# Optimization experiments

Hardware: AMD Instinct MI355X
Metric: run time of the kernel (lower is better)

## Reference

```python
import jax, jax.numpy as jnp
import numpy as np

BETA = 0.01
EPS = 1e-6

def conv3x3(x, w, b):
    y = jax.lax.conv_general_dilated(x, w, (1, 1), 'SAME',
                                     dimension_numbers=('NCHW', 'OIHW', 'NCHW'))
    return y + b[None, :, None, None]

def variance_depth_flow(gt, patch, max_depth):
    B, C, H, W = gt.shape
    py, px = H // patch, W // patch
    # [B,C,py,px,P,P]
    p = gt.reshape(B, C, py, patch, px, patch).transpose(0, 1, 2, 4, 3, 5)
    p = jnp.where((p > 0.1) & (p < max_depth), p, jnp.zeros_like(p))
    bn = jnp.log(p[..., 0, :] + EPS)   # north border  [B,C,py,px,P]
    bs = jnp.log(p[..., -1, :] + EPS)  # south
    bw = jnp.log(p[..., :, 0] + EPS)   # west
    be = jnp.log(p[..., :, -1] + EPS)  # east
    def sx(b):  # shift patches left along x (axis=3), zero-pad last column
        return jnp.concatenate([b[:, :, :, 1:], jnp.zeros_like(b[:, :, :, :1])], axis=3)
    def sy(b):  # shift patches up along y (axis=2), zero-pad last row
        return jnp.concatenate([b[:, :, 1:], jnp.zeros_like(b[:, :, :1])], axis=2)
    diffs = [be - sx(bw), bs - sy(bn), be - sx(be), bs - sy(bs), bw - sx(bw),
             bn - sy(bn), bs - sx(bs), be - sy(be), bn - sx(bn), bw - sy(bw)]
    d = jnp.stack([x.sum(-1) for x in diffs], axis=-1)  # [B,C,py,px,10]
    d = d[:, 0].transpose(0, 3, 1, 2) / patch            # [B,10,py,px]
    return d

def smooth_l1(pred, target, beta):
    d = pred - target
    ad = jnp.abs(d)
    return jnp.where(ad < beta, 0.5 * d * d / beta, ad - 0.5 * beta)

def setup_inputs() -> dict:
    key = jax.random.key(0)
    ks = jax.random.split(key, 7)
    B, FC, DC, hw, HW = 32, 256, 64, 64, 512
    feat = jax.random.normal(ks[0], (B, FC, hw, hw), dtype=jnp.float32)
    depth = jax.random.normal(ks[1], (B, DC, hw, hw), dtype=jnp.float32)
    gts = jax.random.uniform(ks[2], (B, 1, HW, HW), dtype=jnp.float32)
    W_att = jax.random.normal(ks[3], (DC, FC, 3, 3), dtype=jnp.float32) * 0.02
    b_att = jnp.zeros((DC,), dtype=jnp.float32)
    W_post = jax.random.normal(ks[4], (10, DC, 3, 3), dtype=jnp.float32) * 0.05
    b_post = jnp.zeros((10,), dtype=jnp.float32)
    return {"feat": feat, "depth": depth, "gts": gts,
            "W_att": W_att, "b_att": b_att, "W_post": W_post, "b_post": b_post}

def reference(feat, depth, gts, W_att, b_att, W_post, b_post):
    max_depth = 80.0
    n, c, h, w = depth.shape
    patch = gts.shape[2] // h
    flow_gradient = variance_depth_flow(gts, patch, max_depth)  # [B,10,h,w]
    att = jax.nn.sigmoid(conv3x3(feat, W_att, b_att))           # [B,DC,h,w]
    ds = conv3x3(att * depth, W_post, b_post)                   # [B,10,h,w]
    diff = smooth_l1(ds, flow_gradient, BETA)
    return diff.sum() / (h * w * ds.shape[0] * ds.shape[1])
```

## Files before the change

kernel.cpp:

```cpp
#include <hip/hip_runtime.h>
#include <hip/hip_bf16.h>


typedef __attribute__((ext_vector_type(4))) float f32x4;
typedef __attribute__((ext_vector_type(8))) short s16x8;

#define DEVFN __device__ __forceinline__

DEVFN float bf2f(unsigned short u){
  unsigned int x = ((unsigned int)u) << 16;
  float f; __builtin_memcpy(&f, &x, 4); return f;
}
DEVFN unsigned short f2bf(float f){
  unsigned int x; __builtin_memcpy(&x, &f, 4);
  x += 0x7fffu + ((x >> 16) & 1u);
  return (unsigned short)(x >> 16);
}

#define ASYNC16(gp, lp) __builtin_amdgcn_global_load_lds( \
    (const __attribute__((address_space(1))) unsigned int*)(gp), \
    (__attribute__((address_space(3))) unsigned int*)(lp), 16, 0, 0)

__global__ void k_weights(const float* __restrict__ Watt, const float* __restrict__ Wpost,
                          unsigned short* __restrict__ WT1, unsigned short* __restrict__ WT2){
  const int t = blockIdx.x * 256 + threadIdx.x;
  const int n1 = 9 * 64 * 256;
  if (t < n1){
    const int tap = t / (64 * 256);
    const int rem = t % (64 * 256);
    const int oc = rem / 256, ic = rem % 256;
    WT1[t] = f2bf(Watt[(oc * 256 + ic) * 9 + tap]);
  }
  const int n2 = 9 * 16 * 64;
  if (t < n2){
    const int tap = t / (16 * 64);
    const int rem = t % (16 * 64);
    const int od = rem / 64, ic = rem % 64;
    const float v = (od < 10) ? Wpost[(od * 64 + ic) * 9 + tap] : 0.0f;
    WT2[t] = f2bf(v);
  }
}

__global__ void k_borders(const float* __restrict__ gts, float* __restrict__ S,
                          float* __restrict__ out){
  const int bid = blockIdx.x, tid = threadIdx.x;
  if (bid == 0 && tid == 0) *out = 0.0f;
  __shared__ float slab[4096];
  const int rel = bid;
  const float* gp = gts + (size_t)rel * 4096;
#pragma unroll
  for (int it = 0; it < 4; ++it){
    const int id = it * 256 + tid;
    *(f32x4*)&slab[id * 4] = *(const f32x4*)&gp[id * 4];
  }
  __syncthreads();
  const int px = tid & 63, border = tid >> 6;
  float s = 0.0f;
#pragma unroll
  for (int i = 0; i < 8; ++i){
    float v;
    if (border == 0)      v = slab[px * 8 + i];
    else if (border == 1) v = slab[7 * 512 + px * 8 + i];
    else if (border == 2) v = slab[i * 512 + px * 8];
    else                  v = slab[i * 512 + px * 8 + 7];
    v = ((v > 0.1f) && (v < 80.0f)) ? v : 0.0f;
    s += __logf(v + 1e-6f);
  }
  S[((size_t)rel * 64 + px) * 4 + border] = s;
}

__global__ __launch_bounds__(256, 2) void k_gemm1(
    const float* __restrict__ feat,
    const unsigned short* __restrict__ WT1,
    const float* __restrict__ batt,
    const float* __restrict__ depth,
    unsigned short* __restrict__ adT)
{
  __shared__ unsigned short As[6 * 66 * 32];
  __shared__ unsigned short Bs[576 * 32];
  const int t = threadIdx.x;
  const int l = t & 63, w = t >> 6;
  const int b = blockIdx.x >> 4, ytile = blockIdx.x & 15;
  const int y0 = ytile * 4;
  const int fr = l & 15, g = l >> 4;
  const int x = l;

  f32x4 acc[4][4];
#pragma unroll
  for (int i = 0; i < 4; ++i)
#pragma unroll
    for (int j = 0; j < 4; ++j)
#pragma unroll
      for (int q = 0; q < 4; ++q) acc[i][j][q] = 0.0f;

  if (t < 48){
    const int yy = t >> 3, k = t & 7;
    const int xp = (k & 1) ? 65 : 0;
    s16x8 z = {0,0,0,0,0,0,0,0};
    *(s16x8*)&As[(yy * 66 + xp) * 32 + (k >> 1) * 8] = z;
  }

  const int xp = x + 1;
  const int sx = (xp >> 1) & 3;
  const int slotB = (g ^ ((fr >> 1) & 3)) * 8;

  for (int c = 0; c < 8; ++c){
    float rr[48];
#pragma unroll
    for (int j = 0; j < 6; ++j){
      const int yr = y0 - 1 + j;
      if (yr >= 0 && yr < 64){
        const float* gp = feat + ((size_t)(b * 256 + c * 32 + w * 8)) * 4096
                               + (size_t)yr * 64 + x;
#pragma unroll
        for (int e = 0; e < 8; ++e) rr[j * 8 + e] = gp[(size_t)e * 4096];
      } else {
#pragma unroll
        for (int e = 0; e < 8; ++e) rr[j * 8 + e] = 0.0f;
      }
    }
#pragma unroll
    for (int it = 0; it < 9; ++it){
      const int idx = it * 256 + t;
      const int row = idx >> 2;
      const int sg = (idx & 3) ^ ((row >> 1) & 3);
      ASYNC16(WT1 + (size_t)row * 256 + c * 32 + sg * 8, &Bs[(size_t)idx * 8]);
    }
#pragma unroll
    for (int j = 0; j < 6; ++j){
      s16x8 v;
#pragma unroll
      for (int e = 0; e < 8; ++e) v[e] = (short)f2bf(rr[j * 8 + e]);
      *(s16x8*)&As[(j * 66 + xp) * 32 + ((w ^ sx) * 8)] = v;
    }
    __syncthreads();

    for (int tap = 0; tap < 9; ++tap){
      const int dy = tap / 3 - 1, dxp = tap % 3;
      const int r = fr + dxp;
      const int slotA = (g ^ ((r >> 1) & 3)) * 8;
      const int rowb = ((w + dy + 1) * 66 + r) * 32 + slotA;
      s16x8 af[4], bfr[4];
#pragma unroll
      for (int i = 0; i < 4; ++i) af[i] = *(const s16x8*)&As[rowb + i * 512];
#pragma unroll
      for (int j = 0; j < 4; ++j)
        bfr[j] = *(const s16x8*)&Bs[(tap * 64 + j * 16 + fr) * 32 + slotB];
#pragma unroll
      for (int i = 0; i < 4; ++i)
#pragma unroll
        for (int j = 0; j < 4; ++j)
          acc[i][j] = __builtin_amdgcn_mfma_f32_16x16x32_bf16(af[i], bfr[j], acc[i][j], 0, 0, 0);
    }
    __syncthreads();
  }

  const int y = y0 + w;
#pragma unroll
  for (int j = 0; j < 4; ++j){
    const int oc = j * 16 + fr;
    const float bb = batt[oc];
    const float* dpt = depth + ((size_t)(b * 64 + oc)) * 4096 + (size_t)y * 64;
    unsigned short* op = adT + ((size_t)(b * 4096 + y * 64)) * 64 + oc;
#pragma unroll
    for (int i = 0; i < 4; ++i){
#pragma unroll
      for (int q = 0; q < 4; ++q){
        const int xo = i * 16 + g * 4 + q;
        const float v = acc[i][j][q] + bb;
        const float att = 1.0f / (1.0f + __expf(-v));
        op[(size_t)xo * 64] = f2bf(att * dpt[xo]);
      }
    }
  }
}

DEVFN float sel4(f32x4 v, int i){
  const float ab = (i & 1) ? v[1] : v[0];
  const float cd = (i & 1) ? v[3] : v[2];
  return (i & 2) ? cd : ab;
}

__global__ __launch_bounds__(512, 2) void k_gemm2(
    const unsigned short* __restrict__ adT,
    const unsigned short* __restrict__ WT2,
    const float* __restrict__ bpost,
    const f32x4* __restrict__ S,
    float* __restrict__ out)
{
  __shared__ unsigned short As[2][20480];
  __shared__ unsigned short Bs[9216];
  __shared__ float ps[8];
  const int t = threadIdx.x;
  const int l = t & 63, w = t >> 6;
  const int b = blockIdx.x >> 3, ytile = blockIdx.x & 7;
  const int y0 = ytile * 8;
  const int fr = l & 15, g = l >> 4;

  f32x4 acc[4];
#pragma unroll
  for (int i = 0; i < 4; ++i)
#pragma unroll
    for (int q = 0; q < 4; ++q) acc[i][q] = 0.0f;

  auto stageA = [&](int c, int d){
#pragma unroll
    for (int it2 = 0; it2 < 5; ++it2){
      const int it = it2 * 2 + (t >> 8);
      const int yy = y0 - 1 + it;
      const int xx = (t >> 2) & 63, icg = t & 3;
      unsigned short* lp = &As[d][(it * 64 + xx) * 32 + icg * 8];
      if (yy >= 0 && yy < 64){
        const int sg = icg ^ ((xx >> 1) & 3);
        const unsigned short* gp = adT
            + ((size_t)(b * 4096 + yy * 64 + xx)) * 64 + c * 32 + sg * 8;
        ASYNC16(gp, lp);
      } else {
        s16x8 z = {0,0,0,0,0,0,0,0};
        *(s16x8*)lp = z;
      }
    }
  };
#pragma unroll
  for (int it = 0; it < 3; ++it){
    const int idx = it * 512 + t;
    if (idx < 1152){
      const int row = idx >> 3, p = idx & 7;
      const int sg = p ^ (row & 7);
      ASYNC16(WT2 + (size_t)row * 64 + sg * 8, Bs + (size_t)idx * 8);
    }
  }
  stageA(0, 0);
  __syncthreads();

  for (int c = 0; c < 2; ++c){
    if (c == 0) stageA(1, 1);
    const unsigned short* Ab = As[c];
    const int pB = ((c * 4 + g) ^ (fr & 7)) * 8;
    for (int tap = 0; tap < 9; ++tap){
      const int dy = tap / 3 - 1, dx = tap % 3 - 1;
      s16x8 af[4];
#pragma unroll
      for (int i = 0; i < 4; ++i){
        const int xv = i * 16 + fr + dx;
        const bool valid = (xv >= 0) && (xv < 64);
        const int xw = valid ? xv : 0;
        const int slot = (g ^ ((xw >> 1) & 3)) * 8;
        s16x8 v = *(const s16x8*)&Ab[((w + dy + 1) * 64 + xw) * 32 + slot];
        s16x8 z = {0,0,0,0,0,0,0,0};
        af[i] = valid ? v : z;
      }
      const s16x8 bfr = *(const s16x8*)&Bs[(tap * 16 + fr) * 64 + pB];
#pragma unroll
      for (int i = 0; i < 4; ++i)
        acc[i] = __builtin_amdgcn_mfma_f32_16x16x32_bf16(af[i], bfr, acc[i], 0, 0, 0);
    }
    __syncthreads();
  }

  const unsigned aPack = (3u<<0)|(1u<<2)|(3u<<4)|(1u<<6)|(2u<<8)|(0u<<10)|(1u<<12)|(3u<<14)|(0u<<16)|(2u<<18);
  const unsigned bPack = (2u<<0)|(0u<<2)|(3u<<4)|(1u<<6)|(2u<<8)|(0u<<10)|(1u<<12)|(3u<<14)|(0u<<16)|(2u<<18);
  float lsum = 0.0f;
  const int y = y0 + w;
  if (fr < 10){
    const int od = fr;
    const int ai = (aPack >> (2 * od)) & 3;
    const int bi = (bPack >> (2 * od)) & 3;
    const bool xshift = (od & 1) == 0;
    const float bp = bpost[od];
#pragma unroll
    for (int i = 0; i < 4; ++i){
#pragma unroll
      for (int q = 0; q < 4; ++q){
        const int xo = i * 16 + g * 4 + q;
        const size_t gm = (size_t)b * 4096 + (size_t)y * 64 + xo;
        const f32x4 sa = S[gm];
        const bool nb = xshift ? (xo < 63) : (y < 63);
        const size_t ga = xshift ? (nb ? gm + 1 : gm) : (nb ? gm + 64 : gm);
        const f32x4 sbv = S[ga];
        const float sbf = nb ? sel4(sbv, bi) : 0.0f;
        const float flow = (sel4(sa, ai) - sbf) * 0.125f;
        const float dv = acc[i][q] + bp - flow;
        const float adv = fabsf(dv);
        lsum += (adv < 0.01f) ? (50.0f * dv * dv) : (adv - 0.005f);
      }
    }
  }
#pragma unroll
  for (int off = 32; off > 0; off >>= 1) lsum += __shfl_down(lsum, off);
  if (l == 0) ps[w] = lsum;
  __syncthreads();
  if (t == 0){
    float s = 0.0f;
#pragma unroll
    for (int i = 0; i < 8; ++i) s += ps[i];
    atomicAdd(out, s * (1.0f / 1310720.0f));
  }
}

extern "C" void kernel_launch(void* const* d_in, const int* in_sizes, int n_in,
                              void* d_out, int out_size, void* d_ws, size_t ws_size,
                              hipStream_t stream){
  const float* feat  = (const float*)d_in[0];
  const float* depth = (const float*)d_in[1];
  const float* gts   = (const float*)d_in[2];
  const float* Watt  = (const float*)d_in[3];
  const float* batt  = (const float*)d_in[4];
  const float* Wpost = (const float*)d_in[5];
  const float* bpost = (const float*)d_in[6];
  float* out = (float*)d_out;
  char* ws = (char*)d_ws;

  unsigned short* adT = (unsigned short*)ws;
  unsigned short* WT1 = (unsigned short*)(ws + 16777216);
  unsigned short* WT2 = (unsigned short*)(ws + 16777216 + 294912);
  float*          S   = (float*)(ws + 16777216 + 294912 + 18432);

  k_weights<<<576, 256, 0, stream>>>(Watt, Wpost, WT1, WT2);
  k_gemm1<<<512, 256, 0, stream>>>(feat, WT1, batt, depth, adT);
  k_borders<<<2048, 256, 0, stream>>>(gts, S, out);
  k_gemm2<<<256, 512, 0, stream>>>(adT, WT2, bpost, (const f32x4*)S, out);
}
```

Measured before the change: 90.16 us.

## Retile conv GEMM to 8-row tiles with split output channels and vectorized staging

Restructures k_gemm1 so each 512-thread block computes 8 output rows for half of the output channels (32), instead of 4 rows for all 64 channels. Input staging now uses float4 global loads and packed bf16 conversion via v_cvt_pk_bf16_f32 into a new XOR-swizzled LDS layout. The halo overhead per row drops from 6/4 to 10/8, and the per-thread accumulator count halves, which should allow higher occupancy. The cost is that feature-map staging is duplicated across the two channel-half blocks.

```diff
diff --git a/kernel.cpp b/kernel.cpp
--- a/kernel.cpp
+++ b/kernel.cpp
@@ -4,6 +4,7 @@
 
 typedef __attribute__((ext_vector_type(4))) float f32x4;
 typedef __attribute__((ext_vector_type(8))) short s16x8;
+typedef __attribute__((ext_vector_type(4))) unsigned int u32x4;
 
 #define DEVFN __device__ __forceinline__
 
@@ -15,6 +16,11 @@
   unsigned int x; __builtin_memcpy(&x, &f, 4);
   x += 0x7fffu + ((x >> 16) & 1u);
   return (unsigned short)(x >> 16);
+}
+DEVFN unsigned cvtpk(float lo, float hi){
+  unsigned r;
+  asm("v_cvt_pk_bf16_f32 %0, %1, %2" : "=v"(r) : "v"(lo), "v"(hi));
+  return r;
 }
 
 #define ASYNC16(gp, lp) __builtin_amdgcn_global_load_lds( \
@@ -69,87 +75,103 @@
   S[((size_t)rel * 64 + px) * 4 + border] = s;
 }
 
-__global__ __launch_bounds__(256, 2) void k_gemm1(
+__global__ __launch_bounds__(512, 4) void k_gemm1(
     const float* __restrict__ feat,
     const unsigned short* __restrict__ WT1,
     const float* __restrict__ batt,
     const float* __restrict__ depth,
     unsigned short* __restrict__ adT)
 {
-  __shared__ unsigned short As[6 * 66 * 32];
-  __shared__ unsigned short Bs[576 * 32];
+  __shared__ unsigned short As[10 * 33 * 64];
+  __shared__ unsigned short Bs[288 * 32];
   const int t = threadIdx.x;
   const int l = t & 63, w = t >> 6;
-  const int b = blockIdx.x >> 4, ytile = blockIdx.x & 15;
-  const int y0 = ytile * 4;
+  const int bid = blockIdx.x;
+  const int b = bid >> 4, ytile = (bid >> 1) & 7, oh = bid & 1;
+  const int y0 = ytile * 8, oc0 = oh * 32;
   const int fr = l & 15, g = l >> 4;
-  const int x = l;
-
-  f32x4 acc[4][4];
+
+  f32x4 acc[4][2];
 #pragma unroll
   for (int i = 0; i < 4; ++i)
 #pragma unroll
-    for (int j = 0; j < 4; ++j)
+    for (int j = 0; j < 2; ++j)
 #pragma unroll
       for (int q = 0; q < 4; ++q) acc[i][j][q] = 0.0f;
 
-  if (t < 48){
+  if (t < 80){
     const int yy = t >> 3, k = t & 7;
     const int xp = (k & 1) ? 65 : 0;
-    s16x8 z = {0,0,0,0,0,0,0,0};
-    *(s16x8*)&As[(yy * 66 + xp) * 32 + (k >> 1) * 8] = z;
-  }
-
-  const int xp = x + 1;
-  const int sx = (xp >> 1) & 3;
+    const int G = (k >> 1) & 3;
+    const int r = xp >> 1;
+    const int s = (4 * (xp & 1) + G) ^ (r & 7);
+    u32x4 z = {0, 0, 0, 0};
+    *(u32x4*)&As[(yy * 33 + r) * 64 + s * 8] = z;
+  }
+
+  auto stageRow = [&](int c, int yrow){
+    const int yr = y0 - 1 + yrow;
+    f32x4 v[8];
+    if (yr >= 0 && yr < 64){
+      const float* gp = feat + ((size_t)(b * 256 + c * 32 + g * 8)) * 4096
+                             + (size_t)yr * 64 + fr * 4;
+#pragma unroll
+      for (int e = 0; e < 8; ++e) v[e] = *(const f32x4*)(gp + (size_t)e * 4096);
+    } else {
+#pragma unroll
+      for (int e = 0; e < 8; ++e) v[e] = f32x4{0.f, 0.f, 0.f, 0.f};
+    }
+#pragma unroll
+    for (int o = 0; o < 4; ++o){
+      const int xp = fr * 4 + o + 1;
+      u32x4 pk;
+      pk[0] = cvtpk(v[0][o], v[1][o]);
+      pk[1] = cvtpk(v[2][o], v[3][o]);
+      pk[2] = cvtpk(v[4][o], v[5][o]);
+      pk[3] = cvtpk(v[6][o], v[7][o]);
+      const int s = (4 * (xp & 1) + g) ^ ((xp >> 1) & 7);
+      *(u32x4*)&As[((yrow * 33 + (xp >> 1)) * 64 + s * 8)] = pk;
+    }
+  };
+
   const int slotB = (g ^ ((fr >> 1) & 3)) * 8;
 
   for (int c = 0; c < 8; ++c){
-    float rr[48];
-#pragma unroll
-    for (int j = 0; j < 6; ++j){
-      const int yr = y0 - 1 + j;
-      if (yr >= 0 && yr < 64){
-        const float* gp = feat + ((size_t)(b * 256 + c * 32 + w * 8)) * 4096
-                               + (size_t)yr * 64 + x;
-#pragma unroll
-        for (int e = 0; e < 8; ++e) rr[j * 8 + e] = gp[(size_t)e * 4096];
-      } else {
-#pragma unroll
-        for (int e = 0; e < 8; ++e) rr[j * 8 + e] = 0.0f;
-      }
-    }
-#pragma unroll
-    for (int it = 0; it < 9; ++it){
-      const int idx = it * 256 + t;
-      const int row = idx >> 2;
-      const int sg = (idx & 3) ^ ((row >> 1) & 3);
-      ASYNC16(WT1 + (size_t)row * 256 + c * 32 + sg * 8, &Bs[(size_t)idx * 8]);
-    }
-#pragma unroll
-    for (int j = 0; j < 6; ++j){
-      s16x8 v;
-#pragma unroll
-      for (int e = 0; e < 8; ++e) v[e] = (short)f2bf(rr[j * 8 + e]);
-      *(s16x8*)&As[(j * 66 + xp) * 32 + ((w ^ sx) * 8)] = v;
-    }
+#pragma unroll
+    for (int it = 0; it < 3; ++it){
+      const int idx = it * 512 + t;
+      if (idx < 1152){
+        const int rl = idx >> 2;
+        const int tap = rl >> 5, ocl = rl & 31;
+        const int sg = (idx & 3) ^ ((rl >> 1) & 3);
+        ASYNC16(WT1 + (size_t)(tap * 64 + oc0 + ocl) * 256 + c * 32 + sg * 8,
+                &Bs[(size_t)idx * 8]);
+      }
+    }
+    stageRow(c, w);
+    if (w < 2) stageRow(c, 8 + w);
     __syncthreads();
 
+#pragma unroll
     for (int tap = 0; tap < 9; ++tap){
       const int dy = tap / 3 - 1, dxp = tap % 3;
-      const int r = fr + dxp;
-      const int slotA = (g ^ ((r >> 1) & 3)) * 8;
-      const int rowb = ((w + dy + 1) * 66 + r) * 32 + slotA;
-      s16x8 af[4], bfr[4];
-#pragma unroll
-      for (int i = 0; i < 4; ++i) af[i] = *(const s16x8*)&As[rowb + i * 512];
-#pragma unroll
-      for (int j = 0; j < 4; ++j)
-        bfr[j] = *(const s16x8*)&Bs[(tap * 64 + j * 16 + fr) * 32 + slotB];
+      const int yy = w + dy + 1;
+      s16x8 af[4], bfr[2];
+#pragma unroll
+      for (int i = 0; i < 4; ++i){
+        const int xp = i * 16 + fr + dxp;
+        const int s = (4 * (xp & 1) + g) ^ ((xp >> 1) & 7);
+        af[i] = *(const s16x8*)&As[((yy * 33 + (xp >> 1)) * 64 + s * 8)];
+      }
+#pragma unroll
+      for (int j = 0; j < 2; ++j){
+        const int rl = tap * 32 + j * 16 + fr;
+        bfr[j] = *(const s16x8*)&Bs[rl * 32 + slotB];
+      }
 #pragma unroll
       for (int i = 0; i < 4; ++i)
 #pragma unroll
-        for (int j = 0; j < 4; ++j)
+        for (int j = 0; j < 2; ++j)
           acc[i][j] = __builtin_amdgcn_mfma_f32_16x16x32_bf16(af[i], bfr[j], acc[i][j], 0, 0, 0);
     }
     __syncthreads();
@@ -157,8 +179,8 @@
 
   const int y = y0 + w;
 #pragma unroll
-  for (int j = 0; j < 4; ++j){
-    const int oc = j * 16 + fr;
+  for (int j = 0; j < 2; ++j){
+    const int oc = oc0 + j * 16 + fr;
     const float bb = batt[oc];
     const float* dpt = depth + ((size_t)(b * 64 + oc)) * 4096 + (size_t)y * 64;
     unsigned short* op = adT + ((size_t)(b * 4096 + y * 64)) * 64 + oc;
@@ -317,7 +339,7 @@
   float*          S   = (float*)(ws + 16777216 + 294912 + 18432);
 
   k_weights<<<576, 256, 0, stream>>>(Watt, Wpost, WT1, WT2);
-  k_gemm1<<<512, 256, 0, stream>>>(feat, WT1, batt, depth, adT);
+  k_gemm1<<<512, 512, 0, stream>>>(feat, WT1, batt, depth, adT);
   k_borders<<<2048, 256, 0, stream>>>(gts, S, out);
   k_gemm2<<<256, 512, 0, stream>>>(adT, WT2, bpost, (const f32x4*)S, out);
 }
```

After: 108.9 us. +20.8%, slower.

## Double-buffer activation tiles in LDS and read weights directly from global

Applied to the files above, without the earlier changes.

Restructures the k_gemm1 channel loop into a two-stage pipeline. The next chunk's feature loads into registers are issued before the current chunk's MFMA compute and written to the alternate LDS buffer afterward, so one barrier per iteration replaces two. The weight tile no longer goes through LDS; B fragments are read straight from global memory (expected to hit L2) inside each tap. This frees LDS for double buffering, but it adds global-load latency in the MFMA inner loop and more register pressure from the 48-float prefetch buffer.

```diff
diff --git a/kernel.cpp b/kernel.cpp
--- a/kernel.cpp
+++ b/kernel.cpp
@@ -76,8 +76,7 @@
     const float* __restrict__ depth,
     unsigned short* __restrict__ adT)
 {
-  __shared__ unsigned short As[6 * 66 * 32];
-  __shared__ unsigned short Bs[576 * 32];
+  __shared__ unsigned short As[2][6 * 66 * 32];
   const int t = threadIdx.x;
   const int l = t & 63, w = t >> 6;
   const int b = blockIdx.x >> 4, ytile = blockIdx.x & 15;
@@ -93,19 +92,18 @@
 #pragma unroll
       for (int q = 0; q < 4; ++q) acc[i][j][q] = 0.0f;
 
-  if (t < 48){
-    const int yy = t >> 3, k = t & 7;
+  if (t < 96){
+    const int d = t / 48, r = t % 48;
+    const int yy = r >> 3, k = r & 7;
     const int xp = (k & 1) ? 65 : 0;
     s16x8 z = {0,0,0,0,0,0,0,0};
-    *(s16x8*)&As[(yy * 66 + xp) * 32 + (k >> 1) * 8] = z;
+    *(s16x8*)&As[d][(yy * 66 + xp) * 32 + (k >> 1) * 8] = z;
   }
 
   const int xp = x + 1;
   const int sx = (xp >> 1) & 3;
-  const int slotB = (g ^ ((fr >> 1) & 3)) * 8;
-
-  for (int c = 0; c < 8; ++c){
-    float rr[48];
+
+  auto loadA = [&](int c, float* rr){
 #pragma unroll
     for (int j = 0; j < 6; ++j){
       const int yr = y0 - 1 + j;
@@ -119,22 +117,18 @@
         for (int e = 0; e < 8; ++e) rr[j * 8 + e] = 0.0f;
       }
     }
-#pragma unroll
-    for (int it = 0; it < 9; ++it){
-      const int idx = it * 256 + t;
-      const int row = idx >> 2;
-      const int sg = (idx & 3) ^ ((row >> 1) & 3);
-      ASYNC16(WT1 + (size_t)row * 256 + c * 32 + sg * 8, &Bs[(size_t)idx * 8]);
-    }
+  };
+  auto cvtWriteA = [&](int d, const float* rr){
 #pragma unroll
     for (int j = 0; j < 6; ++j){
       s16x8 v;
 #pragma unroll
       for (int e = 0; e < 8; ++e) v[e] = (short)f2bf(rr[j * 8 + e]);
-      *(s16x8*)&As[(j * 66 + xp) * 32 + ((w ^ sx) * 8)] = v;
-    }
-    __syncthreads();
-
+      *(s16x8*)&As[d][(j * 66 + xp) * 32 + ((w ^ sx) * 8)] = v;
+    }
+  };
+  auto compute = [&](const unsigned short* Ab, int c){
+#pragma unroll
     for (int tap = 0; tap < 9; ++tap){
       const int dy = tap / 3 - 1, dxp = tap % 3;
       const int r = fr + dxp;
@@ -142,16 +136,28 @@
       const int rowb = ((w + dy + 1) * 66 + r) * 32 + slotA;
       s16x8 af[4], bfr[4];
 #pragma unroll
-      for (int i = 0; i < 4; ++i) af[i] = *(const s16x8*)&As[rowb + i * 512];
-#pragma unroll
       for (int j = 0; j < 4; ++j)
-        bfr[j] = *(const s16x8*)&Bs[(tap * 64 + j * 16 + fr) * 32 + slotB];
+        bfr[j] = *(const s16x8*)&WT1[(size_t)(tap * 64 + j * 16 + fr) * 256 + c * 32 + g * 8];
+#pragma unroll
+      for (int i = 0; i < 4; ++i) af[i] = *(const s16x8*)&Ab[rowb + i * 512];
 #pragma unroll
       for (int i = 0; i < 4; ++i)
 #pragma unroll
         for (int j = 0; j < 4; ++j)
           acc[i][j] = __builtin_amdgcn_mfma_f32_16x16x32_bf16(af[i], bfr[j], acc[i][j], 0, 0, 0);
     }
+  };
+
+  float rr[48];
+  loadA(0, rr);
+  cvtWriteA(0, rr);
+  __syncthreads();
+
+  for (int c = 0; c < 8; ++c){
+    const int cur = c & 1;
+    if (c < 7) loadA(c + 1, rr);
+    compute(As[cur], c);
+    if (c < 7) cvtWriteA(cur ^ 1, rr);
     __syncthreads();
   }
 
```

After: 128.5 us. 1.43x slower.

## Software-pipeline feat loads in conv1 GEMM with vectorized loads and padded LDS

Applied to the files above, without the earlier changes.

Restructures k_gemm1 so the next channel chunk's feat rows are loaded into registers while the current chunk's MFMAs run, and the weight staging is double-timed after the compute barrier. Feat loads become 16-byte vector loads per lane with packed bf16 conversion via v_cvt_pk_bf16_f32. The A tile in LDS switches from an XOR swizzle to a padded 40-element row stride to avoid bank conflicts. The depth read in the epilogue is vectorized. This raises register pressure from holding two sets of prefetched rows and uses more LDS.

```diff
diff --git a/kernel.cpp b/kernel.cpp
--- a/kernel.cpp
+++ b/kernel.cpp
@@ -4,6 +4,7 @@
 
 typedef __attribute__((ext_vector_type(4))) float f32x4;
 typedef __attribute__((ext_vector_type(8))) short s16x8;
+typedef __attribute__((ext_vector_type(4))) unsigned int u32x4;
 
 #define DEVFN __device__ __forceinline__
 
@@ -15,6 +16,11 @@
   unsigned int x; __builtin_memcpy(&x, &f, 4);
   x += 0x7fffu + ((x >> 16) & 1u);
   return (unsigned short)(x >> 16);
+}
+DEVFN unsigned cvtpk(float lo, float hi){
+  unsigned r;
+  asm("v_cvt_pk_bf16_f32 %0, %1, %2" : "=v"(r) : "v"(lo), "v"(hi));
+  return r;
 }
 
 #define ASYNC16(gp, lp) __builtin_amdgcn_global_load_lds( \
@@ -76,14 +82,13 @@
     const float* __restrict__ depth,
     unsigned short* __restrict__ adT)
 {
-  __shared__ unsigned short As[6 * 66 * 32];
+  __shared__ unsigned short As[6 * 66 * 40];
   __shared__ unsigned short Bs[576 * 32];
   const int t = threadIdx.x;
   const int l = t & 63, w = t >> 6;
   const int b = blockIdx.x >> 4, ytile = blockIdx.x & 15;
   const int y0 = ytile * 4;
   const int fr = l & 15, g = l >> 4;
-  const int x = l;
 
   f32x4 acc[4][4];
 #pragma unroll
@@ -96,29 +101,35 @@
   if (t < 48){
     const int yy = t >> 3, k = t & 7;
     const int xp = (k & 1) ? 65 : 0;
-    s16x8 z = {0,0,0,0,0,0,0,0};
-    *(s16x8*)&As[(yy * 66 + xp) * 32 + (k >> 1) * 8] = z;
-  }
-
-  const int xp = x + 1;
-  const int sx = (xp >> 1) & 3;
-  const int slotB = (g ^ ((fr >> 1) & 3)) * 8;
-
-  for (int c = 0; c < 8; ++c){
-    float rr[48];
-#pragma unroll
-    for (int j = 0; j < 6; ++j){
-      const int yr = y0 - 1 + j;
-      if (yr >= 0 && yr < 64){
-        const float* gp = feat + ((size_t)(b * 256 + c * 32 + w * 8)) * 4096
-                               + (size_t)yr * 64 + x;
-#pragma unroll
-        for (int e = 0; e < 8; ++e) rr[j * 8 + e] = gp[(size_t)e * 4096];
-      } else {
-#pragma unroll
-        for (int e = 0; e < 8; ++e) rr[j * 8 + e] = 0.0f;
-      }
-    }
+    u32x4 z = {0, 0, 0, 0};
+    *(u32x4*)&As[(yy * 66 + xp) * 40 + ((k >> 1) & 3) * 8] = z;
+  }
+
+  auto loadRow = [&](int c, int yy, f32x4* v){
+    const int yr = y0 - 1 + yy;
+    if (yr >= 0 && yr < 64){
+      const float* gp = feat + ((size_t)(b * 256 + c * 32 + g * 8)) * 4096
+                             + (size_t)yr * 64 + fr * 4;
+#pragma unroll
+      for (int e = 0; e < 8; ++e) v[e] = *(const f32x4*)(gp + (size_t)e * 4096);
+    } else {
+#pragma unroll
+      for (int e = 0; e < 8; ++e) v[e] = f32x4{0.f, 0.f, 0.f, 0.f};
+    }
+  };
+  auto cvtWriteRow = [&](int yy, const f32x4* v){
+#pragma unroll
+    for (int o = 0; o < 4; ++o){
+      const int xp = fr * 4 + o + 1;
+      u32x4 pk;
+      pk[0] = cvtpk(v[0][o], v[1][o]);
+      pk[1] = cvtpk(v[2][o], v[3][o]);
+      pk[2] = cvtpk(v[4][o], v[5][o]);
+      pk[3] = cvtpk(v[6][o], v[7][o]);
+      *(u32x4*)&As[(yy * 66 + xp) * 40 + g * 8] = pk;
+    }
+  };
+  auto stageB = [&](int c){
 #pragma unroll
     for (int it = 0; it < 9; ++it){
       const int idx = it * 256 + t;
@@ -126,23 +137,17 @@
       const int sg = (idx & 3) ^ ((row >> 1) & 3);
       ASYNC16(WT1 + (size_t)row * 256 + c * 32 + sg * 8, &Bs[(size_t)idx * 8]);
     }
-#pragma unroll
-    for (int j = 0; j < 6; ++j){
-      s16x8 v;
-#pragma unroll
-      for (int e = 0; e < 8; ++e) v[e] = (short)f2bf(rr[j * 8 + e]);
-      *(s16x8*)&As[(j * 66 + xp) * 32 + ((w ^ sx) * 8)] = v;
-    }
-    __syncthreads();
-
+  };
+  auto compute = [&](){
+    const int slotB = (g ^ ((fr >> 1) & 3)) * 8;
+#pragma unroll
     for (int tap = 0; tap < 9; ++tap){
       const int dy = tap / 3 - 1, dxp = tap % 3;
-      const int r = fr + dxp;
-      const int slotA = (g ^ ((r >> 1) & 3)) * 8;
-      const int rowb = ((w + dy + 1) * 66 + r) * 32 + slotA;
+      const int yy = w + dy + 1;
       s16x8 af[4], bfr[4];
 #pragma unroll
-      for (int i = 0; i < 4; ++i) af[i] = *(const s16x8*)&As[rowb + i * 512];
+      for (int i = 0; i < 4; ++i)
+        af[i] = *(const s16x8*)&As[(yy * 66 + (i * 16 + fr + dxp)) * 40 + g * 8];
 #pragma unroll
       for (int j = 0; j < 4; ++j)
         bfr[j] = *(const s16x8*)&Bs[(tap * 64 + j * 16 + fr) * 32 + slotB];
@@ -151,6 +156,28 @@
 #pragma unroll
         for (int j = 0; j < 4; ++j)
           acc[i][j] = __builtin_amdgcn_mfma_f32_16x16x32_bf16(af[i], bfr[j], acc[i][j], 0, 0, 0);
+    }
+  };
+
+  f32x4 r0[8], r1[8];
+  loadRow(0, w, r0);
+  if (w < 2) loadRow(0, 4 + w, r1);
+  stageB(0);
+  cvtWriteRow(w, r0);
+  if (w < 2) cvtWriteRow(4 + w, r1);
+  __syncthreads();
+
+  for (int c = 0; c < 8; ++c){
+    if (c < 7){
+      loadRow(c + 1, w, r0);
+      if (w < 2) loadRow(c + 1, 4 + w, r1);
+    }
+    compute();
+    __syncthreads();
+    if (c < 7){
+      cvtWriteRow(w, r0);
+      if (w < 2) cvtWriteRow(4 + w, r1);
+      stageB(c + 1);
     }
     __syncthreads();
   }
@@ -164,12 +191,13 @@
     unsigned short* op = adT + ((size_t)(b * 4096 + y * 64)) * 64 + oc;
 #pragma unroll
     for (int i = 0; i < 4; ++i){
+      const f32x4 dv4 = *(const f32x4*)&dpt[i * 16 + g * 4];
 #pragma unroll
       for (int q = 0; q < 4; ++q){
         const int xo = i * 16 + g * 4 + q;
         const float v = acc[i][j][q] + bb;
         const float att = 1.0f / (1.0f + __expf(-v));
-        op[(size_t)xo * 64] = f2bf(att * dpt[xo]);
+        op[(size_t)xo * 64] = f2bf(att * dv4[q]);
       }
     }
   }
```

New measurement: 87.98 us. 1.02x faster.
